# Kernel tuning notes

Hardware: AMD Instinct MI355X
Metric: run time of the kernel (lower is better)

The kernel has to match this reference:

```python
import jax, jax.numpy as jnp
import numpy as np

H, C = 4, 32          # heads, per-head channels (hidden=128)
NEG_SLOPE = 0.2        # PyG GATv2Conv default LeakyReLU slope


def setup_inputs() -> dict:
    key = jax.random.key(0)
    ks = jax.random.split(key, 9)
    N_a, N_m = 100000, 50000     # asset / market node counts
    E_aa, E_am = 600000, 400000  # edge counts per edge type
    D, L = 128, 2                # hidden dims, num GAT layers
    sc = 1.0 / np.sqrt(D).astype(np.float32)

    x_asset = jax.random.normal(ks[0], (N_a, D), jnp.float32)
    x_market = jax.random.normal(ks[1], (N_m, D), jnp.float32)

    edge_aa = jax.random.randint(ks[2], (2, E_aa), 0, N_a, jnp.int32)
    src_am = jax.random.randint(ks[3], (E_am,), 0, N_a, jnp.int32)
    dst_am = jax.random.randint(ks[4], (E_am,), 0, N_m, jnp.int32)
    edge_am = jnp.stack([src_am, dst_am])

    Wl = jax.random.normal(ks[5], (L, D, D), jnp.float32) * sc   # lin_l (src)
    Wr = jax.random.normal(ks[6], (L, D, D), jnp.float32) * sc   # lin_r (dst)
    att = jax.random.normal(ks[7], (L, H, C), jnp.float32) * sc  # attention vector
    bias = jnp.zeros((L, D), jnp.float32)

    return {"x_asset": x_asset, "x_market": x_market,
            "edge_aa": edge_aa, "edge_am": edge_am,
            "Wl": Wl, "Wr": Wr, "att": att, "bias": bias}


def _gatv2(x_src, x_dst, src, dst, Wl, Wr, att, bias):
    """One GATv2Conv: gather-attend-scatter. x_src:[Ns,D], x_dst:[Nd,D]."""
    N_dst = x_dst.shape[0]
    xl = (x_src @ Wl).reshape(-1, H, C)   # transformed src (messages)
    xr = (x_dst @ Wr).reshape(-1, H, C)   # transformed dst
    z = jax.nn.leaky_relu(xl[src] + xr[dst], NEG_SLOPE)     # [E,H,C]
    e = jnp.einsum('ehc,hc->eh', z, att)                    # [E,H] scores
    # softmax over incoming edges per destination node
    m = jax.lax.stop_gradient(jax.ops.segment_max(e, dst, num_segments=N_dst))
    w = jnp.exp(e - m[dst])
    s = jax.ops.segment_sum(w, dst, num_segments=N_dst)
    alpha = w / jnp.maximum(s[dst], jnp.float32(1e-16))     # [E,H]
    out = jax.ops.segment_sum(alpha[..., None] * xl[src], dst, num_segments=N_dst)
    return out.reshape(N_dst, H * C) + bias


def reference(x_asset, x_market, edge_aa, edge_am, Wl, Wr, att, bias):
    # Faithful to source: x_dict is never updated between layers, so every
    # layer reads the ORIGINAL features and only the last layer's dict is kept.
    L = Wl.shape[0]
    out_asset = out_market = None
    for l in range(L):
        out_asset = _gatv2(x_asset, x_asset, edge_aa[0], edge_aa[1],
                           Wl[l], Wr[l], att[l], bias[l])
        out_market = _gatv2(x_asset, x_market, edge_am[0], edge_am[1],
                            Wl[l], Wr[l], att[l], bias[l])
    return out_asset, out_market
```

## Files before the change

### kernel.cpp

```cpp
#include <hip/hip_runtime.h>
#include <hip/hip_bf16.h>


#define NEG_SLOPE 0.2f

typedef __attribute__((ext_vector_type(8))) short short8;
typedef __attribute__((ext_vector_type(4))) float floatx4;
typedef __attribute__((ext_vector_type(4))) unsigned short us4;

__device__ inline unsigned short f2bf(float x) {
    union { float f; unsigned u; } v; v.f = x;
    unsigned r = v.u + 0x7FFF + ((v.u >> 16) & 1);
    return (unsigned short)(r >> 16);
}
__device__ inline float bf2f(unsigned short h) {
    union { unsigned u; float f; } v; v.u = (unsigned)h << 16;
    return v.f;
}

__device__ inline void stage_w(const float* __restrict__ W, unsigned char* lds, int t) {
    const int n = t & 127;
    const int kh = t >> 7;
    unsigned short hb[32], lb[32];
#pragma unroll
    for (int i = 0; i < 32; ++i) {
        int k = kh * 32 + i;
        float w = W[(size_t)k * 128 + n];
        unsigned short h = f2bf(w);
        hb[i] = h;
        lb[i] = f2bf(w - bf2f(h));
    }
#pragma unroll
    for (int j = 0; j < 4; ++j) {
        int k = kh * 32 + j * 8;
        int off = ((n * 256 + k * 2) ^ ((n & 7) << 4));
        short8 hv, lv;
#pragma unroll
        for (int i = 0; i < 8; ++i) { hv[i] = (short)hb[j * 8 + i]; lv[i] = (short)lb[j * 8 + i]; }
        *(short8*)(&lds[off]) = hv;
        *(short8*)(&lds[32768 + off]) = lv;
    }
}

__device__ inline void mfma_pass(const unsigned char* lds, const short8* ah,
                                 const short8* al, int lr, int lkb, floatx4* acc) {
#pragma unroll
    for (int ks = 0; ks < 4; ++ks) {
#pragma unroll
        for (int ct = 0; ct < 8; ++ct) {
            int n = ct * 16 + lr;
            int off = ((n * 256 + (ks * 32 + lkb) * 2) ^ ((n & 7) << 4));
            short8 bh = *(const short8*)(&lds[off]);
            short8 bl = *(const short8*)(&lds[32768 + off]);
            acc[ct] = __builtin_amdgcn_mfma_f32_16x16x32_bf16(ah[ks], bh, acc[ct], 0, 0, 0);
            acc[ct] = __builtin_amdgcn_mfma_f32_16x16x32_bf16(al[ks], bh, acc[ct], 0, 0, 0);
            acc[ct] = __builtin_amdgcn_mfma_f32_16x16x32_bf16(ah[ks], bl, acc[ct], 0, 0, 0);
        }
    }
}

__global__ __launch_bounds__(512) void gemm_all(const float* __restrict__ Xa,
                                                const float* __restrict__ Xm,
                                                const float* __restrict__ Wl,
                                                const float* __restrict__ Wr,
                                                unsigned short* __restrict__ XLb,
                                                float* __restrict__ XR,
                                                const int* __restrict__ aadst,
                                                const int* __restrict__ amdst,
                                                int* __restrict__ deg,
                                                int Eaa, int Eam,
                                                int Na, int Nm, int nblkA) {
    {
        const int stride = gridDim.x * 512;
        const int E = Eaa + Eam;
        for (int e = blockIdx.x * 512 + threadIdx.x; e < E; e += stride) {
            int d = (e < Eaa) ? aadst[e] : (Na + amdst[e - Eaa]);
            atomicAdd(&deg[d], 1);
        }
    }

    __shared__ __align__(16) unsigned char lds[65536];

    const int t = threadIdx.x;
    const int wv = t >> 6;
    const int l = t & 63;
    const int lr = l & 15;
    const int lkb = (l >> 4) * 8;
    const bool isA = ((int)blockIdx.x < nblkA);
    const int blk = isA ? blockIdx.x : blockIdx.x - nblkA;
    const float* __restrict__ X = isA ? Xa : Xm;
    const int M = isA ? Na : Nm;
    const int arow = blk * 128 + wv * 16 + lr;

    short8 ah[4], al[4];
    if (arow < M) {
#pragma unroll
        for (int ks = 0; ks < 4; ++ks) {
            const float* xp = X + (size_t)arow * 128 + ks * 32 + lkb;
            float4 f0 = *(const float4*)xp;
            float4 f1 = *(const float4*)(xp + 4);
            float xv[8] = {f0.x, f0.y, f0.z, f0.w, f1.x, f1.y, f1.z, f1.w};
            short8 h, lo;
#pragma unroll
            for (int i = 0; i < 8; ++i) {
                unsigned short hb = f2bf(xv[i]);
                h[i] = (short)hb;
                lo[i] = (short)f2bf(xv[i] - bf2f(hb));
            }
            ah[ks] = h; al[ks] = lo;
        }
    } else {
#pragma unroll
        for (int ks = 0; ks < 4; ++ks) { ah[ks] = (short8)0; al[ks] = (short8)0; }
    }

    const int orow0 = blk * 128 + wv * 16 + (l >> 4) * 4;
    floatx4 acc[8];

    if (isA) {
        stage_w(Wl, lds, t);
        __syncthreads();
#pragma unroll
        for (int ct = 0; ct < 8; ++ct) acc[ct] = (floatx4)0.f;
        mfma_pass(lds, ah, al, lr, lkb, acc);
#pragma unroll
        for (int ct = 0; ct < 8; ++ct) {
            int col = ct * 16 + lr;
#pragma unroll
            for (int r = 0; r < 4; ++r) {
                int orow = orow0 + r;
                if (orow < M) XLb[(size_t)orow * 128 + col] = f2bf(acc[ct][r]);
            }
        }
        __syncthreads();
        stage_w(Wr, lds, t);
        __syncthreads();
#pragma unroll
        for (int ct = 0; ct < 8; ++ct) acc[ct] = (floatx4)0.f;
        mfma_pass(lds, ah, al, lr, lkb, acc);
#pragma unroll
        for (int ct = 0; ct < 8; ++ct) {
            int col = ct * 16 + lr;
#pragma unroll
            for (int r = 0; r < 4; ++r) {
                int orow = orow0 + r;
                if (orow < M) XR[(size_t)orow * 128 + col] = acc[ct][r];
            }
        }
    } else {
        stage_w(Wr, lds, t);
        __syncthreads();
#pragma unroll
        for (int ct = 0; ct < 8; ++ct) acc[ct] = (floatx4)0.f;
        mfma_pass(lds, ah, al, lr, lkb, acc);
        float* __restrict__ XRm = XR + (size_t)Na * 128;
#pragma unroll
        for (int ct = 0; ct < 8; ++ct) {
            int col = ct * 16 + lr;
#pragma unroll
            for (int r = 0; r < 4; ++r) {
                int orow = orow0 + r;
                if (orow < M) XRm[(size_t)orow * 128 + col] = acc[ct][r];
            }
        }
    }
}

__global__ void alloc_seg(const int* __restrict__ deg, int* __restrict__ row_start,
                          int* __restrict__ fill, int* __restrict__ cursor, int N) {
    int i = blockIdx.x * 256 + threadIdx.x;
    if (i < N) {
        int d = deg[i];
        int r = atomicAdd(cursor, d);
        row_start[i] = r;
        fill[i] = r;
    }
}

__global__ void fillcsr(const int* __restrict__ aasrc, const int* __restrict__ aadst,
                        const int* __restrict__ amsrc, const int* __restrict__ amdst,
                        int* __restrict__ fill, int* __restrict__ csr,
                        int Eaa, int Eam, int Na) {
    const int nqaa = Eaa >> 2, nqam = Eam >> 2;
    int i = blockIdx.x * 256 + threadIdx.x;
    if (i < nqaa) {
        int4 sv = ((const int4*)aasrc)[i];
        int4 dv = ((const int4*)aadst)[i];
        csr[atomicAdd(&fill[dv.x], 1)] = sv.x;
        csr[atomicAdd(&fill[dv.y], 1)] = sv.y;
        csr[atomicAdd(&fill[dv.z], 1)] = sv.z;
        csr[atomicAdd(&fill[dv.w], 1)] = sv.w;
    } else if (i < nqaa + nqam) {
        int4 sv = ((const int4*)amsrc)[i - nqaa];
        int4 dv = ((const int4*)amdst)[i - nqaa];
        csr[atomicAdd(&fill[Na + dv.x], 1)] = sv.x;
        csr[atomicAdd(&fill[Na + dv.y], 1)] = sv.y;
        csr[atomicAdd(&fill[Na + dv.z], 1)] = sv.z;
        csr[atomicAdd(&fill[Na + dv.w], 1)] = sv.w;
    } else {
        int k = i - (nqaa + nqam);
        int remaa = Eaa & 3, remam = Eam & 3;
        if (k < remaa)
            csr[atomicAdd(&fill[aadst[nqaa * 4 + k]], 1)] = aasrc[nqaa * 4 + k];
        else if (k - remaa < remam)
            csr[atomicAdd(&fill[Na + amdst[nqam * 4 + k - remaa]], 1)] = amsrc[nqam * 4 + k - remaa];
    }
}

__global__ __launch_bounds__(256) void gather_gat(const unsigned short* __restrict__ XLb,
                                                  const int* __restrict__ csr,
                                                  const int* __restrict__ row_start,
                                                  const int* __restrict__ deg,
                                                  const float* __restrict__ att,
                                                  const float* __restrict__ bias,
                                                  float* __restrict__ out,
                                                  int Ntot) {
    int wid = (blockIdx.x * 256 + threadIdx.x) >> 6;
    const int l = threadIdx.x & 63;
    if (wid >= Ntot) return;
    const int half = l >> 5;
    const int q = l & 31;

    const float4 av = *(const float4*)(att + (q >> 3) * 32 + (q & 7) * 4);
    const float4 xr = *(const float4*)(out + (size_t)wid * 128 + q * 4);

    const int beg = row_start[wid];
    const int end = beg + deg[wid];
    float s = 0.f;
    float4 acc = make_float4(0.f, 0.f, 0.f, 0.f);

#define EDGE(rv, act)                                                        \
    {                                                                        \
        float x0 = bf2f(rv[0]), x1 = bf2f(rv[1]), x2 = bf2f(rv[2]), x3 = bf2f(rv[3]); \
        float z0 = x0 + xr.x; z0 = fmaxf(z0, NEG_SLOPE * z0);                \
        float z1 = x1 + xr.y; z1 = fmaxf(z1, NEG_SLOPE * z1);                \
        float z2 = x2 + xr.z; z2 = fmaxf(z2, NEG_SLOPE * z2);                \
        float z3 = x3 + xr.w; z3 = fmaxf(z3, NEG_SLOPE * z3);                \
        float p = z0 * av.x;                                                 \
        p = fmaf(z1, av.y, p);                                               \
        p = fmaf(z2, av.z, p);                                               \
        p = fmaf(z3, av.w, p);                                               \
        p += __shfl_xor(p, 1);                                               \
        p += __shfl_xor(p, 2);                                               \
        p += __shfl_xor(p, 4);                                               \
        float w = (act) ? __expf(p) : 0.f;                                   \
        s += w;                                                              \
        acc.x = fmaf(w, x0, acc.x);                                          \
        acc.y = fmaf(w, x1, acc.y);                                          \
        acc.z = fmaf(w, x2, acc.z);                                          \
        acc.w = fmaf(w, x3, acc.w);                                          \
    }

    for (int j = beg; j < end; j += 8) {
        const int b = j + half * 4;
        const bool a0 = (b + 0) < end, a1 = (b + 1) < end,
                   a2 = (b + 2) < end, a3 = (b + 3) < end;
        int s0 = csr[a0 ? b + 0 : beg];
        int s1 = csr[a1 ? b + 1 : beg];
        int s2 = csr[a2 ? b + 2 : beg];
        int s3 = csr[a3 ? b + 3 : beg];
        const us4 r0 = *(const us4*)(XLb + (size_t)s0 * 128 + q * 4);
        const us4 r1 = *(const us4*)(XLb + (size_t)s1 * 128 + q * 4);
        const us4 r2 = *(const us4*)(XLb + (size_t)s2 * 128 + q * 4);
        const us4 r3 = *(const us4*)(XLb + (size_t)s3 * 128 + q * 4);
        EDGE(r0, a0);
        EDGE(r1, a1);
        EDGE(r2, a2);
        EDGE(r3, a3);
    }
#undef EDGE

    s += __shfl_xor(s, 32);
    acc.x += __shfl_xor(acc.x, 32);
    acc.y += __shfl_xor(acc.y, 32);
    acc.z += __shfl_xor(acc.z, 32);
    acc.w += __shfl_xor(acc.w, 32);

    if (half == 0) {
        float inv = 1.f / fmaxf(s, 1e-16f);
        const float4 bv = *(const float4*)(bias + q * 4);
        float4 o = make_float4(fmaf(acc.x, inv, bv.x), fmaf(acc.y, inv, bv.y),
                               fmaf(acc.z, inv, bv.z), fmaf(acc.w, inv, bv.w));
        *(float4*)(out + (size_t)wid * 128 + q * 4) = o;
    }
}

extern "C" void kernel_launch(void* const* d_in, const int* in_sizes, int n_in,
                              void* d_out, int out_size, void* d_ws, size_t ws_size,
                              hipStream_t stream) {
    const float* x_asset  = (const float*)d_in[0];
    const float* x_market = (const float*)d_in[1];
    const int*   eaa      = (const int*)d_in[2];
    const int*   eam      = (const int*)d_in[3];
    const float* Wl       = (const float*)d_in[4];
    const float* Wr       = (const float*)d_in[5];
    const float* att      = (const float*)d_in[6];
    const float* bias     = (const float*)d_in[7];

    const int Na  = in_sizes[0] / 128;
    const int Nm  = in_sizes[1] / 128;
    const int Eaa = in_sizes[2] / 2;
    const int Eam = in_sizes[3] / 2;
    const int Ntot = Na + Nm;

    const float* Wl1   = Wl + 128 * 128;
    const float* Wr1   = Wr + 128 * 128;
    const float* att1  = att + 128;
    const float* bias1 = bias + 128;

    unsigned short* XLb = (unsigned short*)d_ws;
    int*   deg = (int*)(XLb + (size_t)Na * 128);
    int*   cursor = deg + Ntot;
    int*   fill = cursor + 1;
    int*   row_start = fill + Ntot;
    int*   csr = row_start + Ntot;

    float* XR = (float*)d_out;

    hipMemsetAsync(deg, 0, sizeof(int) * (size_t)(Ntot + 1), stream);

    const int nblkA = (Na + 127) / 128;
    const int nblkM = (Nm + 127) / 128;
    gemm_all<<<nblkA + nblkM, 512, 0, stream>>>(x_asset, x_market, Wl1, Wr1,
                                                XLb, XR, eaa + Eaa, eam + Eam,
                                                deg, Eaa, Eam, Na, Nm, nblkA);

    alloc_seg<<<(Ntot + 255) / 256, 256, 0, stream>>>(deg, row_start, fill, cursor, Ntot);

    const int nq = (Eaa >> 2) + (Eam >> 2) + 8;
    fillcsr<<<(nq + 255) / 256, 256, 0, stream>>>(eaa, eaa + Eaa, eam, eam + Eam,
                                                  fill, csr, Eaa, Eam, Na);

    gather_gat<<<(Ntot * 64 + 255) / 256, 256, 0, stream>>>(
        XLb, csr, row_start, deg, att1, bias1, (float*)d_out, Ntot);
}
```

Baseline: 365.7 us.

## Make GEMM persistent with both weights staged once, split degree count

The projection GEMM becomes a persistent kernel of 256 blocks of 1024 threads. Each block stages both Wl and Wr as split-bf16 hi/lo into 128KB of LDS once. Each wave then loops over 16-row chunks of asset and market rows, so the per-block re-staging of weights and the mid-kernel barriers go away. The degree atomics move into a separate vectorised int4 kernel instead of being fused into the GEMM prologue. This adds a kernel launch, and the large LDS footprint and 1024-thread blocks limit occupancy to one block per CU.

```diff
diff --git a/kernel.cpp b/kernel.cpp
--- a/kernel.cpp
+++ b/kernel.cpp
@@ -18,151 +18,159 @@
     return v.f;
 }
 
-__device__ inline void stage_w(const float* __restrict__ W, unsigned char* lds, int t) {
-    const int n = t & 127;
-    const int kh = t >> 7;
-    unsigned short hb[32], lb[32];
-#pragma unroll
-    for (int i = 0; i < 32; ++i) {
-        int k = kh * 32 + i;
-        float w = W[(size_t)k * 128 + n];
-        unsigned short h = f2bf(w);
-        hb[i] = h;
-        lb[i] = f2bf(w - bf2f(h));
-    }
-#pragma unroll
-    for (int j = 0; j < 4; ++j) {
-        int k = kh * 32 + j * 8;
-        int off = ((n * 256 + k * 2) ^ ((n & 7) << 4));
-        short8 hv, lv;
-#pragma unroll
-        for (int i = 0; i < 8; ++i) { hv[i] = (short)hb[j * 8 + i]; lv[i] = (short)lb[j * 8 + i]; }
-        *(short8*)(&lds[off]) = hv;
-        *(short8*)(&lds[32768 + off]) = lv;
-    }
-}
-
-__device__ inline void mfma_pass(const unsigned char* lds, const short8* ah,
-                                 const short8* al, int lr, int lkb, floatx4* acc) {
-#pragma unroll
-    for (int ks = 0; ks < 4; ++ks) {
-#pragma unroll
-        for (int ct = 0; ct < 8; ++ct) {
-            int n = ct * 16 + lr;
-            int off = ((n * 256 + (ks * 32 + lkb) * 2) ^ ((n & 7) << 4));
-            short8 bh = *(const short8*)(&lds[off]);
-            short8 bl = *(const short8*)(&lds[32768 + off]);
-            acc[ct] = __builtin_amdgcn_mfma_f32_16x16x32_bf16(ah[ks], bh, acc[ct], 0, 0, 0);
-            acc[ct] = __builtin_amdgcn_mfma_f32_16x16x32_bf16(al[ks], bh, acc[ct], 0, 0, 0);
-            acc[ct] = __builtin_amdgcn_mfma_f32_16x16x32_bf16(ah[ks], bl, acc[ct], 0, 0, 0);
-        }
-    }
-}
-
-__global__ __launch_bounds__(512) void gemm_all(const float* __restrict__ Xa,
-                                                const float* __restrict__ Xm,
-                                                const float* __restrict__ Wl,
-                                                const float* __restrict__ Wr,
-                                                unsigned short* __restrict__ XLb,
-                                                float* __restrict__ XR,
-                                                const int* __restrict__ aadst,
-                                                const int* __restrict__ amdst,
-                                                int* __restrict__ deg,
-                                                int Eaa, int Eam,
-                                                int Na, int Nm, int nblkA) {
+__global__ __launch_bounds__(1024, 4) void gemm_persist(
+        const float* __restrict__ Xa, const float* __restrict__ Xm,
+        const float* __restrict__ Wl, const float* __restrict__ Wr,
+        unsigned short* __restrict__ XLb, float* __restrict__ XR,
+        int Na, int Nm) {
+    __shared__ __align__(16) unsigned char lds[131072];
+
+    const int t = threadIdx.x;
     {
-        const int stride = gridDim.x * 512;
-        const int E = Eaa + Eam;
-        for (int e = blockIdx.x * 512 + threadIdx.x; e < E; e += stride) {
-            int d = (e < Eaa) ? aadst[e] : (Na + amdst[e - Eaa]);
-            atomicAdd(&deg[d], 1);
-        }
-    }
-
-    __shared__ __align__(16) unsigned char lds[65536];
-
-    const int t = threadIdx.x;
+        const int n = t & 127;
+        const int kh = t >> 7;
+#pragma unroll
+        for (int m = 0; m < 2; ++m) {
+            const float* __restrict__ W = m ? Wr : Wl;
+            const int pbase = m ? 65536 : 0;
+            unsigned short hb[16], lb[16];
+#pragma unroll
+            for (int i = 0; i < 16; ++i) {
+                int k = kh * 16 + i;
+                float w = W[(size_t)k * 128 + n];
+                unsigned short h = f2bf(w);
+                hb[i] = h;
+                lb[i] = f2bf(w - bf2f(h));
+            }
+#pragma unroll
+            for (int j = 0; j < 2; ++j) {
+                int koff = (kh * 16 + j * 8) * 2;
+                int off = pbase + ((n * 256 + koff) ^ ((n & 15) << 4));
+                short8 hv, lv;
+#pragma unroll
+                for (int i = 0; i < 8; ++i) { hv[i] = (short)hb[j * 8 + i]; lv[i] = (short)lb[j * 8 + i]; }
+                *(short8*)(&lds[off]) = hv;
+                *(short8*)(&lds[32768 + off]) = lv;
+            }
+        }
+    }
+    __syncthreads();
+
     const int wv = t >> 6;
     const int l = t & 63;
     const int lr = l & 15;
     const int lkb = (l >> 4) * 8;
-    const bool isA = ((int)blockIdx.x < nblkA);
-    const int blk = isA ? blockIdx.x : blockIdx.x - nblkA;
-    const float* __restrict__ X = isA ? Xa : Xm;
-    const int M = isA ? Na : Nm;
-    const int arow = blk * 128 + wv * 16 + lr;
-
-    short8 ah[4], al[4];
-    if (arow < M) {
+    const int nA = (Na + 15) >> 4;
+    const int nM = (Nm + 15) >> 4;
+    const int nch = nA + nM;
+    const int wstride = gridDim.x * 16;
+
+    for (int c = blockIdx.x * 16 + wv; c < nch; c += wstride) {
+        const bool isA = (c < nA);
+        const float* __restrict__ X = isA ? Xa : Xm;
+        const int M = isA ? Na : Nm;
+        const int row0 = (isA ? c : c - nA) * 16;
+        const int arow = row0 + lr;
+
+        short8 ah[4], al[4];
+        if (arow < M) {
+#pragma unroll
+            for (int ks = 0; ks < 4; ++ks) {
+                const float* xp = X + (size_t)arow * 128 + ks * 32 + lkb;
+                float4 f0 = *(const float4*)xp;
+                float4 f1 = *(const float4*)(xp + 4);
+                float xv[8] = {f0.x, f0.y, f0.z, f0.w, f1.x, f1.y, f1.z, f1.w};
+                short8 h, lo;
+#pragma unroll
+                for (int i = 0; i < 8; ++i) {
+                    unsigned short hb = f2bf(xv[i]);
+                    h[i] = (short)hb;
+                    lo[i] = (short)f2bf(xv[i] - bf2f(hb));
+                }
+                ah[ks] = h; al[ks] = lo;
+            }
+        } else {
+#pragma unroll
+            for (int ks = 0; ks < 4; ++ks) { ah[ks] = (short8)0; al[ks] = (short8)0; }
+        }
+
+        const int or0 = row0 + (l >> 4) * 4;
+        floatx4 acc[8];
+
+#pragma unroll
+        for (int ct = 0; ct < 8; ++ct) acc[ct] = (floatx4)0.f;
 #pragma unroll
         for (int ks = 0; ks < 4; ++ks) {
-            const float* xp = X + (size_t)arow * 128 + ks * 32 + lkb;
-            float4 f0 = *(const float4*)xp;
-            float4 f1 = *(const float4*)(xp + 4);
-            float xv[8] = {f0.x, f0.y, f0.z, f0.w, f1.x, f1.y, f1.z, f1.w};
-            short8 h, lo;
-#pragma unroll
-            for (int i = 0; i < 8; ++i) {
-                unsigned short hb = f2bf(xv[i]);
-                h[i] = (short)hb;
-                lo[i] = (short)f2bf(xv[i] - bf2f(hb));
-            }
-            ah[ks] = h; al[ks] = lo;
-        }
+#pragma unroll
+            for (int ct = 0; ct < 8; ++ct) {
+                int n = ct * 16 + lr;
+                int off = 65536 + ((n * 256 + (ks * 32 + lkb) * 2) ^ ((n & 15) << 4));
+                short8 bh = *(const short8*)(&lds[off]);
+                short8 bl = *(const short8*)(&lds[32768 + off]);
+                acc[ct] = __builtin_amdgcn_mfma_f32_16x16x32_bf16(ah[ks], bh, acc[ct], 0, 0, 0);
+                acc[ct] = __builtin_amdgcn_mfma_f32_16x16x32_bf16(al[ks], bh, acc[ct], 0, 0, 0);
+                acc[ct] = __builtin_amdgcn_mfma_f32_16x16x32_bf16(ah[ks], bl, acc[ct], 0, 0, 0);
+            }
+        }
+        {
+            float* __restrict__ Cb = isA ? XR : (XR + (size_t)Na * 128);
+#pragma unroll
+            for (int ct = 0; ct < 8; ++ct) {
+                int col = ct * 16 + lr;
+#pragma unroll
+                for (int r = 0; r < 4; ++r) {
+                    int orow = or0 + r;
+                    if (orow < M) Cb[(size_t)orow * 128 + col] = acc[ct][r];
+                }
+            }
+        }
+
+        if (isA) {
+#pragma unroll
+            for (int ct = 0; ct < 8; ++ct) acc[ct] = (floatx4)0.f;
+#pragma unroll
+            for (int ks = 0; ks < 4; ++ks) {
+#pragma unroll
+                for (int ct = 0; ct < 8; ++ct) {
+                    int n = ct * 16 + lr;
+                    int off = ((n * 256 + (ks * 32 + lkb) * 2) ^ ((n & 15) << 4));
+                    short8 bh = *(const short8*)(&lds[off]);
+                    short8 bl = *(const short8*)(&lds[32768 + off]);
+                    acc[ct] = __builtin_amdgcn_mfma_f32_16x16x32_bf16(ah[ks], bh, acc[ct], 0, 0, 0);
+                    acc[ct] = __builtin_amdgcn_mfma_f32_16x16x32_bf16(al[ks], bh, acc[ct], 0, 0, 0);
+                    acc[ct] = __builtin_amdgcn_mfma_f32_16x16x32_bf16(ah[ks], bl, acc[ct], 0, 0, 0);
+                }
+            }
+#pragma unroll
+            for (int ct = 0; ct < 8; ++ct) {
+                int col = ct * 16 + lr;
+#pragma unroll
+                for (int r = 0; r < 4; ++r) {
+                    int orow = or0 + r;
+                    if (orow < M) XLb[(size_t)orow * 128 + col] = f2bf(acc[ct][r]);
+                }
+            }
+        }
+    }
+}
+
+__global__ void degcount(const int* __restrict__ aadst, const int* __restrict__ amdst,
+                         int* __restrict__ deg, int Eaa, int Eam, int Na) {
+    const int nqaa = Eaa >> 2, nqam = Eam >> 2;
+    int i = blockIdx.x * 256 + threadIdx.x;
+    if (i < nqaa) {
+        int4 d = ((const int4*)aadst)[i];
+        atomicAdd(&deg[d.x], 1); atomicAdd(&deg[d.y], 1);
+        atomicAdd(&deg[d.z], 1); atomicAdd(&deg[d.w], 1);
+    } else if (i < nqaa + nqam) {
+        int4 d = ((const int4*)amdst)[i - nqaa];
+        atomicAdd(&deg[Na + d.x], 1); atomicAdd(&deg[Na + d.y], 1);
+        atomicAdd(&deg[Na + d.z], 1); atomicAdd(&deg[Na + d.w], 1);
     } else {
-#pragma unroll
-        for (int ks = 0; ks < 4; ++ks) { ah[ks] = (short8)0; al[ks] = (short8)0; }
-    }
-
-    const int orow0 = blk * 128 + wv * 16 + (l >> 4) * 4;
-    floatx4 acc[8];
-
-    if (isA) {
-        stage_w(Wl, lds, t);
-        __syncthreads();
-#pragma unroll
-        for (int ct = 0; ct < 8; ++ct) acc[ct] = (floatx4)0.f;
-        mfma_pass(lds, ah, al, lr, lkb, acc);
-#pragma unroll
-        for (int ct = 0; ct < 8; ++ct) {
-            int col = ct * 16 + lr;
-#pragma unroll
-            for (int r = 0; r < 4; ++r) {
-                int orow = orow0 + r;
-                if (orow < M) XLb[(size_t)orow * 128 + col] = f2bf(acc[ct][r]);
-            }
-        }
-        __syncthreads();
-        stage_w(Wr, lds, t);
-        __syncthreads();
-#pragma unroll
-        for (int ct = 0; ct < 8; ++ct) acc[ct] = (floatx4)0.f;
-        mfma_pass(lds, ah, al, lr, lkb, acc);
-#pragma unroll
-        for (int ct = 0; ct < 8; ++ct) {
-            int col = ct * 16 + lr;
-#pragma unroll
-            for (int r = 0; r < 4; ++r) {
-                int orow = orow0 + r;
-                if (orow < M) XR[(size_t)orow * 128 + col] = acc[ct][r];
-            }
-        }
-    } else {
-        stage_w(Wr, lds, t);
-        __syncthreads();
-#pragma unroll
-        for (int ct = 0; ct < 8; ++ct) acc[ct] = (floatx4)0.f;
-        mfma_pass(lds, ah, al, lr, lkb, acc);
-        float* __restrict__ XRm = XR + (size_t)Na * 128;
-#pragma unroll
-        for (int ct = 0; ct < 8; ++ct) {
-            int col = ct * 16 + lr;
-#pragma unroll
-            for (int r = 0; r < 4; ++r) {
-                int orow = orow0 + r;
-                if (orow < M) XRm[(size_t)orow * 128 + col] = acc[ct][r];
-            }
-        }
+        int k = i - (nqaa + nqam);
+        int remaa = Eaa & 3, remam = Eam & 3;
+        if (k < remaa) atomicAdd(&deg[aadst[nqaa * 4 + k]], 1);
+        else if (k - remaa < remam) atomicAdd(&deg[Na + amdst[nqam * 4 + k - remaa]], 1);
     }
 }
 
@@ -319,15 +327,14 @@
 
     hipMemsetAsync(deg, 0, sizeof(int) * (size_t)(Ntot + 1), stream);
 
-    const int nblkA = (Na + 127) / 128;
-    const int nblkM = (Nm + 127) / 128;
-    gemm_all<<<nblkA + nblkM, 512, 0, stream>>>(x_asset, x_market, Wl1, Wr1,
-                                                XLb, XR, eaa + Eaa, eam + Eam,
-                                                deg, Eaa, Eam, Na, Nm, nblkA);
+    const int nq = (Eaa >> 2) + (Eam >> 2) + 8;
+    degcount<<<(nq + 255) / 256, 256, 0, stream>>>(eaa + Eaa, eam + Eam, deg, Eaa, Eam, Na);
+
+    gemm_persist<<<256, 1024, 0, stream>>>(x_asset, x_market, Wl1, Wr1,
+                                           XLb, XR, Na, Nm);
 
     alloc_seg<<<(Ntot + 255) / 256, 256, 0, stream>>>(deg, row_start, fill, cursor, Ntot);
 
-    const int nq = (Eaa >> 2) + (Eam >> 2) + 8;
     fillcsr<<<(nq + 255) / 256, 256, 0, stream>>>(eaa, eaa + Eaa, eam, eam + Eam,
                                                   fill, csr, Eaa, Eam, Na);
 
```

Result: slower. 599.5 us (+63.9%).
